# Optimization experiments

Hardware: AMD Instinct MI355X
Metric: run time of the kernel (lower is better)

## Reference

```python
import jax, jax.numpy as jnp
import numpy as np

BATCH, N_IN, N_OUT = 1024, 512, 512
GRID, DEGREE = 8, 3
NUM_BASIS = GRID + DEGREE  # 11
LO, HI = -3.0, 3.0
_h = (HI - LO) / GRID
# extended knot vector: GRID + 2*DEGREE + 1 knots -> GRID + DEGREE basis functions
KNOTS = jnp.asarray(np.linspace(LO - DEGREE * _h, HI + DEGREE * _h,
                                GRID + 2 * DEGREE + 1), dtype=jnp.float32)


def bspline_basis(x):
    """Cox-de Boor recursion. x: (batch, n_in) -> (batch, n_in, NUM_BASIS)."""
    t = KNOTS
    xb = x[..., None]
    B = ((xb >= t[:-1]) & (xb < t[1:])).astype(x.dtype)  # degree 0
    for d in range(1, DEGREE + 1):
        left = (xb - t[:-(d + 1)]) / (t[d:-1] - t[:-(d + 1)])
        right = (t[d + 1:] - xb) / (t[d + 1:] - t[1:-d])
        B = left * B[..., :-1] + right * B[..., 1:]
    return B


def setup_inputs() -> dict:
    key = jax.random.key(0)
    kx, kc, kw = jax.random.split(key, 3)
    x = jax.random.normal(kx, (BATCH, N_IN), dtype=jnp.float32)
    # xavier_normal_ init for c: fan_in = num_basis, fan_out = n_in*n_out
    c_std = float(np.sqrt(2.0 / (N_IN * N_OUT + NUM_BASIS)))
    c = jax.random.normal(kc, (N_IN * N_OUT, NUM_BASIS), dtype=jnp.float32) * c_std
    w_std = float(np.sqrt(2.0 / (N_IN + N_OUT)))
    w = jax.random.normal(kw, (N_IN, N_OUT), dtype=jnp.float32) * w_std
    return {"x": x, "c": c, "w": w}


def reference(x, c, w):
    # spline basis: (batch, n_in, K)
    bx = bspline_basis(x)
    # per-edge coefficients: (n_in, n_out, K)
    cr = c.reshape(N_IN, N_OUT, NUM_BASIS)
    # out[b,i,o] = sum_k bx[b,i,k] * c[i,o,k]
    spline = jnp.einsum('bik,iok->bio', bx, cr)
    # w * (silu(x) + spline), summed over n_in -> (batch, n_out)
    out = jnp.einsum('io,bio->bo', w, jax.nn.silu(x)[..., None] + spline)
    return out
```

## Files before the change

### kernel.cpp

```cpp
#include <hip/hip_runtime.h>

#define BATCH 1024
#define NIN   512
#define NOUT  512
#define NB    11
#define KDIM  (NIN * 12)
#define SPLITS 16
#define IPS    (NIN / SPLITS)
#define LDW    104

typedef short bf16x8 __attribute__((ext_vector_type(8)));
typedef float f32x4  __attribute__((ext_vector_type(4)));
typedef unsigned short ushort8 __attribute__((ext_vector_type(8)));

__device__ __forceinline__ unsigned short f2bf(float f) {
  unsigned u = __float_as_uint(f);
  u += 0x7fff + ((u >> 16) & 1);
  return (unsigned short)(u >> 16);
}
__device__ __forceinline__ float bf2f(unsigned short h) {
  return __uint_as_float((unsigned)h << 16);
}

__global__ __launch_bounds__(256) void k_prep(const float* __restrict__ c,
                                              const float* __restrict__ w,
                                              unsigned short* __restrict__ Bt) {
  __shared__ float          ws_[4 * 128];
  __shared__ unsigned short sbt[128 * 48];
  int tid = threadIdx.x;
  int bc  = blockIdx.x;
  int i0  = (bc >> 2) * 4;
  int o0  = (bc & 3) * 128;
  if (tid < 128) {
    int il = tid >> 5, oq = (tid & 31) * 4;
    *(f32x4*)&ws_[il * 128 + oq] = *(const f32x4*)&w[(size_t)(i0 + il) * NOUT + o0 + oq];
  }
  __syncthreads();
  for (int n = 0; n < 6; ++n) {
    int ch = n * 256 + tid;
    if (ch < 1408) {
      int il  = ch / 352;
      int off = (ch - il * 352) * 4;
      f32x4 cv = *(const f32x4*)&c[(size_t)(i0 + il) * (NIN * NB) + (size_t)o0 * NB + off];
#pragma unroll
      for (int e = 0; e < 4; ++e) {
        int t  = off + e;
        int op = t / 11;
        int k  = t - op * 11;
        sbt[op * 48 + il * 12 + k] = f2bf(cv[e] * ws_[il * 128 + op]);
      }
    }
  }
#pragma unroll
  for (int e = 0; e < 2; ++e) {
    int idx = e * 256 + tid;
    int op = idx >> 2, il = idx & 3;
    sbt[op * 48 + il * 12 + 11] = f2bf(ws_[il * 128 + op]);
  }
  __syncthreads();
  for (int n = 0; n < 3; ++n) {
    int ch = n * 256 + tid;
    int op = ch / 6, q = ch - op * 6;
    *(ushort8*)&Bt[(size_t)(o0 + op) * KDIM + i0 * 12 + q * 8] =
        *(const ushort8*)&sbt[op * 48 + q * 8];
  }
}

__device__ __forceinline__ void a_gen(f32x4 xv, unsigned short* __restrict__ As,
                                      int tid) {
  int bl  = tid >> 1;
  int il0 = (tid & 1) * 4;
  unsigned short* arow = &As[bl * LDW];
#pragma unroll
  for (int q = 0; q < 4; ++q) {
    int col = (il0 + q) * 12;
    *(unsigned long long*)&arow[col]     = 0ULL;
    *(unsigned long long*)&arow[col + 4] = 0ULL;
    *(unsigned long long*)&arow[col + 8] = 0ULL;
    float xq = xv[q];
    float um = (xq + 5.25f) * (1.0f / 0.75f);
    int   m  = (int)floorf(um);
    if (m >= 0 && m <= 13) {
      float u  = um - (float)m;
      float u2 = u * u, u3 = u2 * u;
      float omu = 1.0f - u;
      float w3 = u3 * (1.0f / 6.0f);
      float w2 = (-3.0f*u3 + 3.0f*u2 + 3.0f*u + 1.0f) * (1.0f/6.0f);
      float w1 = (3.0f*u3 - 6.0f*u2 + 4.0f) * (1.0f/6.0f);
      float w0 = omu * omu * omu * (1.0f / 6.0f);
      int j0 = m - 3;
      if (j0 >= 0 && j0 <= 10)         arow[col + j0]     = f2bf(w0);
      if (j0 + 1 >= 0 && j0 + 1 <= 10) arow[col + j0 + 1] = f2bf(w1);
      if (j0 + 2 >= 0 && j0 + 2 <= 10) arow[col + j0 + 2] = f2bf(w2);
      if (m <= 10)                     arow[col + m]      = f2bf(w3);
    }
    float sig = 1.0f / (1.0f + __expf(-xq));
    arow[col + 11] = f2bf(xq * sig);
  }
}

__global__ __launch_bounds__(256) void k_fused(const float* __restrict__ x,
                                               const unsigned short* __restrict__ Bt,
                                               unsigned short* __restrict__ part,
                                               float* __restrict__ out,
                                               int splits, int ipersplit) {
  __shared__ unsigned short As[128 * LDW];
  __shared__ unsigned short Bs[128 * LDW];
  const int tid  = threadIdx.x;
  const int lane = tid & 63, wave = tid >> 6;
  const int wr = wave >> 1, wc = wave & 1;
  const int mbase = blockIdx.x * 128, nbase = blockIdx.y * 128;
  const int split = blockIdx.z;
  const int istart = split * ipersplit;

  f32x4 acc[4][4] = {};
  const int mrow = lane & 15;
  const int kq   = (lane >> 4) * 8;

  const float* xg = &x[(size_t)(mbase + (tid >> 1)) * NIN + (tid & 1) * 4];
  int brow[6], bcg[6];
  const unsigned short* bg[6];
#pragma unroll
  for (int n = 0; n < 6; ++n) {
    int ch  = n * 256 + tid;
    brow[n] = ch / 12;
    bcg[n]  = ch - brow[n] * 12;
    bg[n]   = &Bt[(size_t)(nbase + brow[n]) * KDIM + bcg[n] * 8];
  }

  const int iters = ipersplit / 8;
  f32x4   xv = *(const f32x4*)&xg[istart];
  ushort8 bv[6];
#pragma unroll
  for (int n = 0; n < 6; ++n) bv[n] = *(const ushort8*)&bg[n][(size_t)istart * 12];

  for (int it = 0; it < iters; ++it) {
    int ib = istart + it * 8;
    a_gen(xv, As, tid);
#pragma unroll
    for (int n = 0; n < 6; ++n)
      *(ushort8*)&Bs[brow[n] * LDW + bcg[n] * 8] = bv[n];

    if (it + 1 < iters) {
      int ibn = ib + 8;
      xv = *(const f32x4*)&xg[ibn];
#pragma unroll
      for (int n = 0; n < 6; ++n) bv[n] = *(const ushort8*)&bg[n][(size_t)ibn * 12];
    }
    __syncthreads();

#pragma unroll
    for (int ks = 0; ks < 96; ks += 32) {
      bf16x8 af[4], bfr[4];
#pragma unroll
      for (int mt = 0; mt < 4; ++mt)
        af[mt] = *(const bf16x8*)&As[(wr * 64 + mt * 16 + mrow) * LDW + ks + kq];
#pragma unroll
      for (int nt = 0; nt < 4; ++nt)
        bfr[nt] = *(const bf16x8*)&Bs[(wc * 64 + nt * 16 + mrow) * LDW + ks + kq];
#pragma unroll
      for (int mt = 0; mt < 4; ++mt)
#pragma unroll
        for (int nt = 0; nt < 4; ++nt)
          acc[mt][nt] = __builtin_amdgcn_mfma_f32_16x16x32_bf16(af[mt], bfr[nt], acc[mt][nt], 0, 0, 0);
    }
    __syncthreads();
  }

  const int rq = (lane >> 4) * 4;
  if (splits == 1) {
#pragma unroll
    for (int mt = 0; mt < 4; ++mt)
#pragma unroll
      for (int nt = 0; nt < 4; ++nt) {
        int colg = nbase + wc * 64 + nt * 16 + mrow;
#pragma unroll
        for (int r = 0; r < 4; ++r) {
          int rowg = mbase + wr * 64 + mt * 16 + rq + r;
          out[(size_t)rowg * NOUT + colg] = acc[mt][nt][r];
        }
      }
    return;
  }
#pragma unroll
  for (int mt = 0; mt < 4; ++mt)
#pragma unroll
    for (int nt = 0; nt < 4; ++nt) {
      int colg = nbase + wc * 64 + nt * 16 + mrow;
#pragma unroll
      for (int r = 0; r < 4; ++r) {
        int rowg = mbase + wr * 64 + mt * 16 + rq + r;
        part[((size_t)split * BATCH + rowg) * NOUT + colg] = f2bf(acc[mt][nt][r]);
      }
    }
}

__global__ __launch_bounds__(256) void k_reduce(const unsigned short* __restrict__ part,
                                                float* __restrict__ out) {
  int t = blockIdx.x * 256 + threadIdx.x;
  const ushort8* pv = (const ushort8*)part;
  float s[8] = {};
#pragma unroll
  for (int sp = 0; sp < SPLITS; ++sp) {
    ushort8 v = pv[(size_t)sp * (BATCH * NOUT / 8) + t];
#pragma unroll
    for (int e = 0; e < 8; ++e) s[e] += bf2f(v[e]);
  }
  f32x4 lo = { s[0], s[1], s[2], s[3] };
  f32x4 hi = { s[4], s[5], s[6], s[7] };
  ((f32x4*)out)[t * 2]     = lo;
  ((f32x4*)out)[t * 2 + 1] = hi;
}

extern "C" void kernel_launch(void* const* d_in, const int* in_sizes, int n_in,
                              void* d_out, int out_size, void* d_ws, size_t ws_size,
                              hipStream_t stream) {
  const float* x = (const float*)d_in[0];
  const float* c = (const float*)d_in[1];
  const float* w = (const float*)d_in[2];
  float* out = (float*)d_out;

  unsigned short* Bt = (unsigned short*)d_ws;
  size_t off_part = (size_t)NOUT * KDIM * 2;
  unsigned short* part = (unsigned short*)((char*)d_ws + off_part);
  size_t need = off_part + (size_t)SPLITS * BATCH * NOUT * 2;

  k_prep<<<dim3(512), 256, 0, stream>>>(c, w, Bt);
  if (ws_size >= need) {
    k_fused<<<dim3(8, 4, SPLITS), 256, 0, stream>>>(x, Bt, part, out, SPLITS, IPS);
    k_reduce<<<dim3((BATCH * NOUT / 8) / 256), 256, 0, stream>>>(part, out);
  } else {
    k_fused<<<dim3(8, 4, 1), 256, 0, stream>>>(x, Bt, part, out, 1, NIN);
  }
}
```

Baseline: 89.20 us.

## Load B fragments straight from global and double-buffer A tile in LDS

The B (coefficient) tile is no longer staged through shared memory. Each wave loads its MFMA B fragments directly from global memory into registers, rotating between two register sets so the next k-slice is prefetched during the current MFMA group. The A tile generated from the spline basis is double-buffered in LDS, so only one barrier per iteration is needed and the next A tile is built while the current MFMAs run. The trade-off is that B is fetched twice (once by each wave row) through strided global/L2 accesses, and those loads expose more latency than the old shared-memory staging.

```diff
diff --git a/kernel.cpp b/kernel.cpp
--- a/kernel.cpp
+++ b/kernel.cpp
@@ -99,13 +99,56 @@
   }
 }
 
+__device__ __forceinline__ void mfma_group(const unsigned short* __restrict__ asb,
+                                           const bf16x8 (&bfr)[4],
+                                           f32x4 (&acc)[4][4],
+                                           int wr, int mrow, int kq, int ks) {
+  bf16x8 af[4];
+#pragma unroll
+  for (int mt = 0; mt < 4; ++mt)
+    af[mt] = *(const bf16x8*)&asb[(wr * 64 + mt * 16 + mrow) * LDW + ks + kq];
+#pragma unroll
+  for (int mt = 0; mt < 4; ++mt)
+#pragma unroll
+    for (int nt = 0; nt < 4; ++nt)
+      acc[mt][nt] = __builtin_amdgcn_mfma_f32_16x16x32_bf16(af[mt], bfr[nt], acc[mt][nt], 0, 0, 0);
+}
+
+__device__ __forceinline__ void iter_body(int it, int iters, int istart,
+                                          const unsigned short* __restrict__ asb,
+                                          unsigned short* __restrict__ asn,
+                                          bf16x8 (&bcur)[4], bf16x8 (&bnxt)[4],
+                                          const unsigned short* const (&bptr)[4],
+                                          const float* __restrict__ xg, f32x4& xv,
+                                          f32x4 (&acc)[4][4],
+                                          int tid, int wr, int mrow, int kq) {
+  const int ib = istart + it * 8;
+  const int kb = ib * 12;
+#pragma unroll
+  for (int nt = 0; nt < 4; ++nt) bnxt[nt] = *(const bf16x8*)&bptr[nt][kb + 32];
+  mfma_group(asb, bcur, acc, wr, mrow, kq, 0);
+#pragma unroll
+  for (int nt = 0; nt < 4; ++nt) bcur[nt] = *(const bf16x8*)&bptr[nt][kb + 64];
+  mfma_group(asb, bnxt, acc, wr, mrow, kq, 32);
+  if (it + 1 < iters) {
+    const int kbn = (ib + 8) * 12;
+#pragma unroll
+    for (int nt = 0; nt < 4; ++nt) bnxt[nt] = *(const bf16x8*)&bptr[nt][kbn];
+  }
+  mfma_group(asb, bcur, acc, wr, mrow, kq, 64);
+  if (it + 1 < iters) {
+    a_gen(xv, asn, tid);
+    if (it + 2 < iters) xv = *(const f32x4*)&xg[ib + 16];
+    __syncthreads();
+  }
+}
+
 __global__ __launch_bounds__(256) void k_fused(const float* __restrict__ x,
                                                const unsigned short* __restrict__ Bt,
                                                unsigned short* __restrict__ part,
                                                float* __restrict__ out,
                                                int splits, int ipersplit) {
-  __shared__ unsigned short As[128 * LDW];
-  __shared__ unsigned short Bs[128 * LDW];
+  __shared__ unsigned short As2[2][128 * LDW];
   const int tid  = threadIdx.x;
   const int lane = tid & 63, wave = tid >> 6;
   const int wr = wave >> 1, wc = wave & 1;
@@ -117,54 +160,29 @@
   const int mrow = lane & 15;
   const int kq   = (lane >> 4) * 8;
 
+  const unsigned short* bptr[4];
+#pragma unroll
+  for (int nt = 0; nt < 4; ++nt)
+    bptr[nt] = &Bt[(size_t)(nbase + wc * 64 + nt * 16 + mrow) * KDIM + kq];
+
   const float* xg = &x[(size_t)(mbase + (tid >> 1)) * NIN + (tid & 1) * 4];
-  int brow[6], bcg[6];
-  const unsigned short* bg[6];
-#pragma unroll
-  for (int n = 0; n < 6; ++n) {
-    int ch  = n * 256 + tid;
-    brow[n] = ch / 12;
-    bcg[n]  = ch - brow[n] * 12;
-    bg[n]   = &Bt[(size_t)(nbase + brow[n]) * KDIM + bcg[n] * 8];
-  }
 
   const int iters = ipersplit / 8;
-  f32x4   xv = *(const f32x4*)&xg[istart];
-  ushort8 bv[6];
-#pragma unroll
-  for (int n = 0; n < 6; ++n) bv[n] = *(const ushort8*)&bg[n][(size_t)istart * 12];
-
-  for (int it = 0; it < iters; ++it) {
-    int ib = istart + it * 8;
-    a_gen(xv, As, tid);
-#pragma unroll
-    for (int n = 0; n < 6; ++n)
-      *(ushort8*)&Bs[brow[n] * LDW + bcg[n] * 8] = bv[n];
-
-    if (it + 1 < iters) {
-      int ibn = ib + 8;
-      xv = *(const f32x4*)&xg[ibn];
-#pragma unroll
-      for (int n = 0; n < 6; ++n) bv[n] = *(const ushort8*)&bg[n][(size_t)ibn * 12];
-    }
-    __syncthreads();
-
-#pragma unroll
-    for (int ks = 0; ks < 96; ks += 32) {
-      bf16x8 af[4], bfr[4];
-#pragma unroll
-      for (int mt = 0; mt < 4; ++mt)
-        af[mt] = *(const bf16x8*)&As[(wr * 64 + mt * 16 + mrow) * LDW + ks + kq];
-#pragma unroll
-      for (int nt = 0; nt < 4; ++nt)
-        bfr[nt] = *(const bf16x8*)&Bs[(wc * 64 + nt * 16 + mrow) * LDW + ks + kq];
-#pragma unroll
-      for (int mt = 0; mt < 4; ++mt)
-#pragma unroll
-        for (int nt = 0; nt < 4; ++nt)
-          acc[mt][nt] = __builtin_amdgcn_mfma_f32_16x16x32_bf16(af[mt], bfr[nt], acc[mt][nt], 0, 0, 0);
-    }
-    __syncthreads();
+
+  f32x4 xv = *(const f32x4*)&xg[istart];
+  a_gen(xv, As2[0], tid);
+  if (iters > 1) xv = *(const f32x4*)&xg[istart + 8];
+  bf16x8 bA[4], bB[4];
+  {
+    const int kb = istart * 12;
+#pragma unroll
+    for (int nt = 0; nt < 4; ++nt) bA[nt] = *(const bf16x8*)&bptr[nt][kb];
+  }
+  __syncthreads();
+
+  for (int it = 0; it < iters; it += 2) {
+    iter_body(it,     iters, istart, As2[0], As2[1], bA, bB, bptr, xg, xv, acc, tid, wr, mrow, kq);
+    iter_body(it + 1, iters, istart, As2[1], As2[0], bB, bA, bptr, xg, xv, acc, tid, wr, mrow, kq);
   }
 
   const int rq = (lane >> 4) * 4;
```

After: 93.28 us. +4.6%, slower.
